# Kernel tuning notes

Measured on AMD Instinct MI355X. Metric: run time of the kernel, lower is better.

The kernel has to match this reference:

```python
import jax, jax.numpy as jnp
import numpy as np

B, S, D = 4, 2048, 2048


def setup_inputs() -> dict:
    key = jax.random.key(0)
    ks = jax.random.split(key, 9)
    scale = 1.0 / np.sqrt(D)
    x = jax.random.normal(ks[0], (B, S, D), dtype=jnp.float32)
    # causal mask, broadcast to [B, S, S]; 0 -> masked
    mask = jnp.broadcast_to(jnp.tril(jnp.ones((S, S), dtype=jnp.int32)), (B, S, S))
    Wq = jax.random.normal(ks[1], (D, D), dtype=jnp.float32) * scale
    Wk = jax.random.normal(ks[2], (D, D), dtype=jnp.float32) * scale
    Wv = jax.random.normal(ks[3], (D, D), dtype=jnp.float32) * scale
    Wp = jax.random.normal(ks[4], (D, D), dtype=jnp.float32) * scale
    bq = jnp.zeros((D,), jnp.float32)
    bk = jnp.zeros((D,), jnp.float32)
    bv = jnp.zeros((D,), jnp.float32)
    bp = jnp.zeros((D,), jnp.float32)
    return {"x": x, "mask": mask, "Wq": Wq, "bq": bq, "Wk": Wk, "bk": bk,
            "Wv": Wv, "bv": bv, "Wp": Wp, "bp": bp}


def reference(x, mask, Wq, bq, Wk, bk, Wv, bv, Wp, bp):
    # single-head scaled dot-product attention (cache=None path, eval mode)
    d_k = x.shape[-1]
    inv_std = 1.0 / jnp.sqrt(jnp.asarray(d_k, x.dtype))
    q = jnp.einsum('bsd,ed->bse', x, Wq) + bq  # nn.Linear: x @ W^T + b
    k = jnp.einsum('bsd,ed->bse', x, Wk) + bk
    v = jnp.einsum('bsd,ed->bse', x, Wv) + bv
    scores = jnp.einsum('bqd,bkd->bqk', q, k) * inv_std  # [B,S,S]
    scores = jnp.where(mask == 0, jnp.asarray(-jnp.inf, scores.dtype), scores)
    attn = jax.nn.softmax(scores, axis=-1)
    ctx = jnp.einsum('bqk,bkd->bqd', attn, v)
    out = jnp.einsum('bsd,ed->bse', ctx, Wp) + bp
    return out
```

## Files before the change

kernel.cpp:

```cpp
#include <hip/hip_runtime.h>
#include <hip/hip_bf16.h>
#include <type_traits>
#include <math.h>


typedef __bf16 bf16x8_t __attribute__((ext_vector_type(8)));
typedef float f32x4_t __attribute__((ext_vector_type(4)));
typedef unsigned short u16x8_t __attribute__((ext_vector_type(8)));

#define BM 128
#define BN 128
#define BK 64

__device__ inline unsigned short f2bf(float f) {
  unsigned int u = __builtin_bit_cast(unsigned int, f);
  unsigned int r = u + 0x7fffu + ((u >> 16) & 1u);
  return (unsigned short)(r >> 16);
}

__device__ inline void gl2lds16(const unsigned short* g, unsigned short* l) {
  __builtin_amdgcn_global_load_lds(
      (const __attribute__((address_space(1))) unsigned int*)g,
      (__attribute__((address_space(3))) unsigned int*)l, 16, 0, 0);
}

__global__ __launch_bounds__(256) void cast_f32_bf16(
    const float* __restrict__ in, unsigned short* __restrict__ out, long n4) {
  long i = blockIdx.x * 256L + threadIdx.x;
  if (i >= n4) return;
  float4 f = ((const float4*)in)[i];
  ushort4 u;
  u.x = f2bf(f.x); u.y = f2bf(f.y); u.z = f2bf(f.z); u.w = f2bf(f.w);
  ((ushort4*)out)[i] = u;
}

__global__ __launch_bounds__(256) void cast_w4(
    const float* __restrict__ w0, const float* __restrict__ w1,
    const float* __restrict__ w2, const float* __restrict__ w3,
    unsigned short* __restrict__ o0, unsigned short* __restrict__ o1,
    unsigned short* __restrict__ o2, unsigned short* __restrict__ o3,
    long n4) {
  long i = blockIdx.x * 256L + threadIdx.x;
  if (i >= n4) return;
  const float* in; unsigned short* out;
  switch (blockIdx.y) {
    case 0: in = w0; out = o0; break;
    case 1: in = w1; out = o1; break;
    case 2: in = w2; out = o2; break;
    default: in = w3; out = o3; break;
  }
  float4 f = ((const float4*)in)[i];
  ushort4 u;
  u.x = f2bf(f.x); u.y = f2bf(f.y); u.z = f2bf(f.z); u.w = f2bf(f.w);
  ((ushort4*)out)[i] = u;
}

#define GEMM_PROLOGUE()                                                        \
  const int tid = threadIdx.x;                                                 \
  const int lane = tid & 63;                                                   \
  const int wave = tid >> 6;                                                   \
  const int wm = (wave >> 1) * 64;                                             \
  const int wn = (wave & 1) * 64;                                              \
  __shared__ unsigned short smem[2 * BM * BK];                      \
  unsigned short* As = smem;                                                   \
  unsigned short* Bs = smem + BM * BK;                                         \
  const int lr = lane >> 3;                                                    \
  const int swcol = ((lane & 7) ^ lr) * 8;                                     \
  const int cbase = wave * 4;                                                  \
  f32x4_t acc[4][4] = {};                                                      \
  const int fr = lane & 15;                                                    \
  const int q4 = lane >> 4;                                                    \
  const int fo0 = ((q4 ^ (fr & 7)) * 8);             \
  const int fo1 = (((q4 + 4) ^ (fr & 7)) * 8);

#define GEMM_KLOOP(Ab, Bb, K, Keff)                                            \
  for (int k0 = 0; k0 < (Keff); k0 += BK) {                                    \
    __syncthreads();                                                           \
    _Pragma("unroll")                                                          \
    for (int i = 0; i < 4; i++) {                                              \
      const int c = cbase + i;                                                 \
      gl2lds16((Ab) + (size_t)(c * 8 + lr) * (K) + k0 + swcol, As + c * 512);  \
      gl2lds16((Bb) + (size_t)(c * 8 + lr) * (K) + k0 + swcol, Bs + c * 512);  \
    }                                                                          \
    __syncthreads();                                                           \
    {                                                                          \
      bf16x8_t af[4], bfv[4];                                                  \
      _Pragma("unroll")                                                        \
      for (int mi = 0; mi < 4; mi++)                                           \
        af[mi] = __builtin_bit_cast(                                           \
            bf16x8_t, *(const u16x8_t*)&As[(wm + mi * 16 + fr) * BK + fo0]);   \
      _Pragma("unroll")                                                        \
      for (int ni = 0; ni < 4; ni++)                                           \
        bfv[ni] = __builtin_bit_cast(                                          \
            bf16x8_t, *(const u16x8_t*)&Bs[(wn + ni * 16 + fr) * BK + fo0]);   \
      _Pragma("unroll")                                                        \
      for (int mi = 0; mi < 4; mi++)                                           \
        _Pragma("unroll")                                                      \
        for (int ni = 0; ni < 4; ni++)                                         \
          acc[mi][ni] = __builtin_amdgcn_mfma_f32_16x16x32_bf16(               \
              af[mi], bfv[ni], acc[mi][ni], 0, 0, 0);                          \
      _Pragma("unroll")                                                        \
      for (int mi = 0; mi < 4; mi++)                                           \
        af[mi] = __builtin_bit_cast(                                           \
            bf16x8_t, *(const u16x8_t*)&As[(wm + mi * 16 + fr) * BK + fo1]);   \
      _Pragma("unroll")                                                        \
      for (int ni = 0; ni < 4; ni++)                                           \
        bfv[ni] = __builtin_bit_cast(                                          \
            bf16x8_t, *(const u16x8_t*)&Bs[(wn + ni * 16 + fr) * BK + fo1]);   \
      _Pragma("unroll")                                                        \
      for (int mi = 0; mi < 4; mi++)                                           \
        _Pragma("unroll")                                                      \
        for (int ni = 0; ni < 4; ni++)                                         \
          acc[mi][ni] = __builtin_amdgcn_mfma_f32_16x16x32_bf16(               \
              af[mi], bfv[ni], acc[mi][ni], 0, 0, 0);                          \
    }                                                                          \
  }

template <int MODE, typename OutT>
__global__ __launch_bounds__(256) void gemm_nt(
    const unsigned short* __restrict__ A, const unsigned short* __restrict__ B,
    OutT* __restrict__ C, const float* __restrict__ bias, float alpha,
    int M, int N, int K, size_t sA, size_t sB, size_t sC) {
  const int bm = blockIdx.y * BM;
  const int bn = blockIdx.x * BN;
  if (MODE == 1 && bn >= bm + BM) return;
  int Keff = K;
  if (MODE == 2) { int kl = bm + BM; Keff = kl < K ? kl : K; }

  A += (size_t)blockIdx.z * sA;
  B += (size_t)blockIdx.z * sB;
  C += (size_t)blockIdx.z * sC;

  GEMM_PROLOGUE();
  const unsigned short* Ab = A + (size_t)bm * K;
  const unsigned short* Bb = B + (size_t)bn * K;
  GEMM_KLOOP(Ab, Bb, K, Keff);

  const int cr = (lane >> 4) * 4;
  const int cc = lane & 15;
#pragma unroll
  for (int ni = 0; ni < 4; ni++) {
    const int col = bn + wn + ni * 16 + cc;
    const float bs = bias ? bias[col] : 0.f;
#pragma unroll
    for (int mi = 0; mi < 4; mi++) {
      const int row = bm + wm + mi * 16 + cr;
#pragma unroll
      for (int r = 0; r < 4; r++) {
        float v = acc[mi][ni][r] * alpha + bs;
        if constexpr (std::is_same_v<OutT, float>)
          C[(size_t)(row + r) * N + col] = v;
        else
          C[(size_t)(row + r) * N + col] = f2bf(v);
      }
    }
  }
}

__global__ __launch_bounds__(256) void gemm_qkv(
    const unsigned short* __restrict__ A, const unsigned short* __restrict__ Bw,
    unsigned short* __restrict__ Q, unsigned short* __restrict__ Kd,
    unsigned short* __restrict__ Vt,
    const float* __restrict__ bq, const float* __restrict__ bk,
    const float* __restrict__ bv, int K, int D, int S) {
  const int bm = blockIdx.y * BM;
  const int bn = blockIdx.x * BN;

  GEMM_PROLOGUE();
  const unsigned short* Ab = A + (size_t)bm * K;
  const unsigned short* Bb = Bw + (size_t)bn * K;
  GEMM_KLOOP(Ab, Bb, K, K);

  const int cr = (lane >> 4) * 4;
  const int cc = lane & 15;
#pragma unroll
  for (int ni = 0; ni < 4; ni++) {
    const int col = bn + wn + ni * 16 + cc;
    const int sel = col >> 11;
    const int idx = col & (D - 1);
    const float bs = (sel == 0 ? bq : sel == 1 ? bk : bv)[idx];
#pragma unroll
    for (int mi = 0; mi < 4; mi++) {
      const int row = bm + wm + mi * 16 + cr;
      if (sel < 2) {
        unsigned short* dst = sel == 0 ? Q : Kd;
#pragma unroll
        for (int r = 0; r < 4; r++)
          dst[(size_t)(row + r) * D + idx] = f2bf(acc[mi][ni][r] + bs);
      } else {
        const int b = row >> 11;
        const int s = row & (S - 1);
        ushort4 pack;
        pack.x = f2bf(acc[mi][ni][0] + bs);
        pack.y = f2bf(acc[mi][ni][1] + bs);
        pack.z = f2bf(acc[mi][ni][2] + bs);
        pack.w = f2bf(acc[mi][ni][3] + bs);
        *(ushort4*)&Vt[(size_t)b * D * S + (size_t)idx * S + s] = pack;
      }
    }
  }
}

__global__ __launch_bounds__(256) void softmax_causal(
    const float* __restrict__ Sc, unsigned short* __restrict__ P, int n) {
  const int row = blockIdx.x;
  const int q = row & (n - 1);
  const float* srow = Sc + (size_t)row * n;
  unsigned short* prow = P + (size_t)row * n;
  const int tid = threadIdx.x, lane = tid & 63, wid = tid >> 6;
  __shared__ float red[4];

  float m = -3.0e38f;
  for (int j = tid; j <= q; j += 256) m = fmaxf(m, srow[j]);
#pragma unroll
  for (int o = 32; o; o >>= 1) m = fmaxf(m, __shfl_down(m, o, 64));
  if (lane == 0) red[wid] = m;
  __syncthreads();
  m = fmaxf(fmaxf(red[0], red[1]), fmaxf(red[2], red[3]));
  __syncthreads();

  float s = 0.f;
  for (int j = tid; j <= q; j += 256) s += __expf(srow[j] - m);
#pragma unroll
  for (int o = 32; o; o >>= 1) s += __shfl_down(s, o, 64);
  if (lane == 0) red[wid] = s;
  __syncthreads();
  s = red[0] + red[1] + red[2] + red[3];
  const float inv = 1.f / s;

  for (int j = tid; j < n; j += 256) {
    float v = (j <= q) ? __expf(srow[j] - m) * inv : 0.f;
    prow[j] = f2bf(v);
  }
}

extern "C" void kernel_launch(void* const* d_in, const int* in_sizes, int n_in,
                              void* d_out, int out_size, void* d_ws, size_t ws_size,
                              hipStream_t stream) {
  const int B = 4, S = 2048, D = 2048;
  const int M = B * S;

  const float* x  = (const float*)d_in[0];
  const float* Wq = (const float*)d_in[2];
  const float* bq = (const float*)d_in[3];
  const float* Wk = (const float*)d_in[4];
  const float* bk = (const float*)d_in[5];
  const float* Wv = (const float*)d_in[6];
  const float* bv = (const float*)d_in[7];
  const float* Wp = (const float*)d_in[8];
  const float* bp = (const float*)d_in[9];
  float* out = (float*)d_out;

  char* ws = (char*)d_ws;
  const size_t MB = 1ull << 20;
  unsigned short* xb   = (unsigned short*)(ws + 0);
  unsigned short* wqkv = (unsigned short*)(ws + 32 * MB);
  unsigned short* wpb  = (unsigned short*)(ws + 56 * MB);
  unsigned short* qb   = (unsigned short*)(ws + 64 * MB);
  unsigned short* kb   = (unsigned short*)(ws + 96 * MB);
  unsigned short* vtb  = (unsigned short*)(ws + 160 * MB);
  float*          sc   = (float*)(ws + 192 * MB);
  unsigned short* pb   = qb;
  unsigned short* cb   = kb;

  const long nx = (long)M * D;
  const long nw = (long)D * D;

  cast_f32_bf16<<<dim3((unsigned)((nx / 4 + 255) / 256)), 256, 0, stream>>>(x, xb, nx / 4);
  cast_w4<<<dim3((unsigned)((nw / 4 + 255) / 256), 4), 256, 0, stream>>>(
      Wq, Wk, Wv, Wp,
      wqkv, wqkv + (size_t)D * D, wqkv + 2 * (size_t)D * D, wpb, nw / 4);

  const dim3 blk(256);

  gemm_qkv<<<dim3(3 * D / BN, M / BM), blk, 0, stream>>>(
      xb, wqkv, qb, kb, vtb, bq, bk, bv, D, D, S);

  const float inv_std = 1.f / sqrtf((float)D);
  gemm_nt<1, float><<<dim3(S / BN, S / BM, B), blk, 0, stream>>>(
      qb, kb, sc, nullptr, inv_std, S, S, D, (size_t)S * D, (size_t)S * D, (size_t)S * S);

  softmax_causal<<<dim3(B * S), blk, 0, stream>>>(sc, pb, S);

  gemm_nt<2, unsigned short><<<dim3(D / BN, S / BM, B), blk, 0, stream>>>(
      pb, vtb, cb, nullptr, 1.f, S, D, S, (size_t)S * S, (size_t)D * S, (size_t)S * D);

  gemm_nt<0, float><<<dim3(D / BN, M / BM), blk, 0, stream>>>(
      cb, wpb, out, bp, 1.f, M, D, D, 0, 0, 0);
}
```

Baseline: 682.9 us.

## Replace 128x128 GEMMs with 256x256 tiles using a double-buffered, interleaved load/MFMA pipeline

Swaps all GEMM kernels for a 256x256 tile, 512-thread version. Each block double-buffers its LDS tiles, interleaving global-to-LDS prefetch of the next K tiles with MFMA compute phases, using explicit waitcnt, sched barriers and setprio. It also remaps workgroup IDs in an XCD-aware way to improve L2 locality. Larger tiles raise data reuse and hide memory latency, at the cost of more registers and 128KB of LDS per block, and of coarser causal skipping in the QK^T and PV GEMMs.

```diff
diff --git a/kernel.cpp b/kernel.cpp
--- a/kernel.cpp
+++ b/kernel.cpp
@@ -8,10 +8,6 @@
 typedef float f32x4_t __attribute__((ext_vector_type(4)));
 typedef unsigned short u16x8_t __attribute__((ext_vector_type(8)));
 
-#define BM 128
-#define BN 128
-#define BK 64
-
 __device__ inline unsigned short f2bf(float f) {
   unsigned int u = __builtin_bit_cast(unsigned int, f);
   unsigned int r = u + 0x7fffu + ((u >> 16) & 1u);
@@ -23,6 +19,19 @@
       (const __attribute__((address_space(1))) unsigned int*)g,
       (__attribute__((address_space(3))) unsigned int*)l, 16, 0, 0);
 }
+
+__device__ __forceinline__ bf16x8_t ldf(const unsigned short* p) {
+  return __builtin_bit_cast(bf16x8_t, *(const u16x8_t*)p);
+}
+
+#define MF(a_, b_, c_) \
+  (c_) = __builtin_amdgcn_mfma_f32_16x16x32_bf16((a_), (b_), (c_), 0, 0, 0)
+#define FENCE() asm volatile("" ::: "memory")
+#define BAR() __builtin_amdgcn_s_barrier()
+#define LGK0() asm volatile("s_waitcnt lgkmcnt(0)" ::: "memory")
+#define VM6() asm volatile("s_waitcnt vmcnt(6)" ::: "memory")
+#define SCHED0() __builtin_amdgcn_sched_barrier(0)
+#define PRIO(x) __builtin_amdgcn_s_setprio(x)
 
 __global__ __launch_bounds__(256) void cast_f32_bf16(
     const float* __restrict__ in, unsigned short* __restrict__ out, long n4) {
@@ -55,99 +64,174 @@
   ((ushort4*)out)[i] = u;
 }
 
-#define GEMM_PROLOGUE()                                                        \
-  const int tid = threadIdx.x;                                                 \
-  const int lane = tid & 63;                                                   \
-  const int wave = tid >> 6;                                                   \
-  const int wm = (wave >> 1) * 64;                                             \
-  const int wn = (wave & 1) * 64;                                              \
-  __shared__ unsigned short smem[2 * BM * BK];                      \
-  unsigned short* As = smem;                                                   \
-  unsigned short* Bs = smem + BM * BK;                                         \
-  const int lr = lane >> 3;                                                    \
-  const int swcol = ((lane & 7) ^ lr) * 8;                                     \
-  const int cbase = wave * 4;                                                  \
-  f32x4_t acc[4][4] = {};                                                      \
-  const int fr = lane & 15;                                                    \
-  const int q4 = lane >> 4;                                                    \
-  const int fo0 = ((q4 ^ (fr & 7)) * 8);             \
-  const int fo1 = (((q4 + 4) ^ (fr & 7)) * 8);
-
-#define GEMM_KLOOP(Ab, Bb, K, Keff)                                            \
-  for (int k0 = 0; k0 < (Keff); k0 += BK) {                                    \
-    __syncthreads();                                                           \
-    _Pragma("unroll")                                                          \
-    for (int i = 0; i < 4; i++) {                                              \
-      const int c = cbase + i;                                                 \
-      gl2lds16((Ab) + (size_t)(c * 8 + lr) * (K) + k0 + swcol, As + c * 512);  \
-      gl2lds16((Bb) + (size_t)(c * 8 + lr) * (K) + k0 + swcol, Bs + c * 512);  \
-    }                                                                          \
-    __syncthreads();                                                           \
-    {                                                                          \
-      bf16x8_t af[4], bfv[4];                                                  \
-      _Pragma("unroll")                                                        \
-      for (int mi = 0; mi < 4; mi++)                                           \
-        af[mi] = __builtin_bit_cast(                                           \
-            bf16x8_t, *(const u16x8_t*)&As[(wm + mi * 16 + fr) * BK + fo0]);   \
-      _Pragma("unroll")                                                        \
-      for (int ni = 0; ni < 4; ni++)                                           \
-        bfv[ni] = __builtin_bit_cast(                                          \
-            bf16x8_t, *(const u16x8_t*)&Bs[(wn + ni * 16 + fr) * BK + fo0]);   \
-      _Pragma("unroll")                                                        \
-      for (int mi = 0; mi < 4; mi++)                                           \
-        _Pragma("unroll")                                                      \
-        for (int ni = 0; ni < 4; ni++)                                         \
-          acc[mi][ni] = __builtin_amdgcn_mfma_f32_16x16x32_bf16(               \
-              af[mi], bfv[ni], acc[mi][ni], 0, 0, 0);                          \
-      _Pragma("unroll")                                                        \
-      for (int mi = 0; mi < 4; mi++)                                           \
-        af[mi] = __builtin_bit_cast(                                           \
-            bf16x8_t, *(const u16x8_t*)&As[(wm + mi * 16 + fr) * BK + fo1]);   \
-      _Pragma("unroll")                                                        \
-      for (int ni = 0; ni < 4; ni++)                                           \
-        bfv[ni] = __builtin_bit_cast(                                          \
-            bf16x8_t, *(const u16x8_t*)&Bs[(wn + ni * 16 + fr) * BK + fo1]);   \
-      _Pragma("unroll")                                                        \
-      for (int mi = 0; mi < 4; mi++)                                           \
-        _Pragma("unroll")                                                      \
-        for (int ni = 0; ni < 4; ni++)                                         \
-          acc[mi][ni] = __builtin_amdgcn_mfma_f32_16x16x32_bf16(               \
-              af[mi], bfv[ni], acc[mi][ni], 0, 0, 0);                          \
-    }                                                                          \
-  }
+__device__ __forceinline__ void g256_kloop(
+    const unsigned short* __restrict__ A, const unsigned short* __restrict__ B,
+    int K, int Keff, unsigned short* smem, f32x4_t (&acc)[8][4]) {
+  const int tid = threadIdx.x;
+  const int lane = tid & 63;
+  const int wave = tid >> 6;
+  const int wr = wave >> 2;
+  const int wc = wave & 3;
+  const int fr = lane & 15;
+  const int q4 = lane >> 4;
+  const int s0 = (q4 ^ (fr & 7)) * 8;
+  const int s1 = ((q4 + 4) ^ (fr & 7)) * 8;
+  const size_t rowK =
+      (size_t)(wave * 8 + (lane >> 3)) * (size_t)K +
+      (size_t)(((lane & 7) ^ ((lane >> 3) & 7)) * 8);
+  const size_t K64 = (size_t)64 * K;
+  const size_t K128 = (size_t)128 * K;
+  const int wofs = wave * 512;
+  const int NT = Keff >> 6;
+
+#define STG(gp_, lh_)                        \
+  do {                                       \
+    const unsigned short* g_ = (gp_) + rowK; \
+    gl2lds16(g_, (lh_) + wofs);              \
+    gl2lds16(g_ + K64, (lh_) + 4096 + wofs); \
+  } while (0)
+
+  STG(A, smem);
+  STG(A + K128, smem + 8192);
+  STG(B, smem + 16384);
+  STG(B + K128, smem + 24576);
+  STG(B + 64, smem + 32768 + 16384);
+  STG(B + K128 + 64, smem + 32768 + 24576);
+  STG(A + 64, smem + 32768);
+  VM6();
+  FENCE();
+  BAR();
+
+  for (int kt = 0; kt < NT; ++kt) {
+    unsigned short* bc = smem + ((kt & 1) << 15);
+    unsigned short* nb = smem + (((kt + 1) & 1) << 15);
+    const unsigned short* Ahc = bc + wr * 8192 + fr * 64;
+    const unsigned short* Bhc =
+        bc + 16384 + (wc >> 1) * 8192 + (wc & 1) * 4096 + fr * 64;
+    int k1 = (kt + 1) << 6; if (k1 >= Keff) k1 -= Keff;
+    int k2 = (kt + 2) << 6; if (k2 >= Keff) k2 -= Keff;
+
+    bf16x8_t bfr[4][2], af01[2][2], af25[4][2], af67[2][2];
+
+#pragma unroll
+    for (int n = 0; n < 4; ++n) {
+      const unsigned short* p = Bhc + n * 1024;
+      bfr[n][0] = ldf(p + s0);
+      bfr[n][1] = ldf(p + s1);
+    }
+#pragma unroll
+    for (int m = 0; m < 2; ++m) {
+      const unsigned short* p = Ahc + m * 1024;
+      af01[m][0] = ldf(p + s0);
+      af01[m][1] = ldf(p + s1);
+    }
+    STG(A + K128 + k1, nb + 8192);
+    FENCE(); BAR(); LGK0(); SCHED0();
+    PRIO(1);
+#pragma unroll
+    for (int m = 0; m < 2; ++m)
+#pragma unroll
+      for (int n = 0; n < 4; ++n) {
+        MF(af01[m][0], bfr[n][0], acc[m][n]);
+        MF(af01[m][1], bfr[n][1], acc[m][n]);
+      }
+    PRIO(0);
+    FENCE(); BAR();
+
+#pragma unroll
+    for (int m = 0; m < 4; ++m) {
+      const unsigned short* p = Ahc + (m + 2) * 1024;
+      af25[m][0] = ldf(p + s0);
+      af25[m][1] = ldf(p + s1);
+    }
+    STG(B + k2, bc + 16384);
+    FENCE(); BAR(); LGK0(); SCHED0();
+    PRIO(1);
+#pragma unroll
+    for (int m = 0; m < 2; ++m)
+#pragma unroll
+      for (int n = 0; n < 4; ++n) {
+        MF(af25[m][0], bfr[n][0], acc[2 + m][n]);
+        MF(af25[m][1], bfr[n][1], acc[2 + m][n]);
+      }
+    PRIO(0);
+    FENCE(); BAR();
+
+#pragma unroll
+    for (int m = 0; m < 2; ++m) {
+      const unsigned short* p = Ahc + (m + 6) * 1024;
+      af67[m][0] = ldf(p + s0);
+      af67[m][1] = ldf(p + s1);
+    }
+    STG(B + K128 + k2, bc + 24576);
+    FENCE(); BAR(); LGK0(); SCHED0();
+    PRIO(1);
+#pragma unroll
+    for (int m = 0; m < 2; ++m)
+#pragma unroll
+      for (int n = 0; n < 4; ++n) {
+        MF(af25[2 + m][0], bfr[n][0], acc[4 + m][n]);
+        MF(af25[2 + m][1], bfr[n][1], acc[4 + m][n]);
+      }
+    PRIO(0);
+    FENCE(); BAR();
+
+    STG(A + k2, bc);
+    FENCE(); BAR(); LGK0(); SCHED0();
+    PRIO(1);
+#pragma unroll
+    for (int m = 0; m < 2; ++m)
+#pragma unroll
+      for (int n = 0; n < 4; ++n) {
+        MF(af67[m][0], bfr[n][0], acc[6 + m][n]);
+        MF(af67[m][1], bfr[n][1], acc[6 + m][n]);
+      }
+    PRIO(0);
+    VM6();
+    FENCE(); BAR();
+  }
+#undef STG
+}
 
 template <int MODE, typename OutT>
-__global__ __launch_bounds__(256) void gemm_nt(
+__global__ __launch_bounds__(512, 2) void gemm256_nt(
     const unsigned short* __restrict__ A, const unsigned short* __restrict__ B,
     OutT* __restrict__ C, const float* __restrict__ bias, float alpha,
-    int M, int N, int K, size_t sA, size_t sB, size_t sC) {
-  const int bm = blockIdx.y * BM;
-  const int bn = blockIdx.x * BN;
-  if (MODE == 1 && bn >= bm + BM) return;
+    int N, int K, size_t sA, size_t sB, size_t sC) {
+  int lin = blockIdx.y * gridDim.x + blockIdx.x;
+  const int nwg = gridDim.x * gridDim.y;
+  lin = (lin & 7) * (nwg >> 3) + (lin >> 3);
+  const int bm = (lin / gridDim.x) * 256;
+  const int bn = (lin % gridDim.x) * 256;
+  if (MODE == 1 && bn >= bm + 256) return;
   int Keff = K;
-  if (MODE == 2) { int kl = bm + BM; Keff = kl < K ? kl : K; }
-
-  A += (size_t)blockIdx.z * sA;
-  B += (size_t)blockIdx.z * sB;
+  if (MODE == 2) { int kl = bm + 256; Keff = kl < K ? kl : K; }
+
+  A += (size_t)blockIdx.z * sA + (size_t)bm * K;
+  B += (size_t)blockIdx.z * sB + (size_t)bn * K;
   C += (size_t)blockIdx.z * sC;
 
-  GEMM_PROLOGUE();
-  const unsigned short* Ab = A + (size_t)bm * K;
-  const unsigned short* Bb = B + (size_t)bn * K;
-  GEMM_KLOOP(Ab, Bb, K, Keff);
-
-  const int cr = (lane >> 4) * 4;
-  const int cc = lane & 15;
-#pragma unroll
-  for (int ni = 0; ni < 4; ni++) {
-    const int col = bn + wn + ni * 16 + cc;
+  __shared__ unsigned short smem[65536];
+  f32x4_t acc[8][4] = {};
+  g256_kloop(A, B, K, Keff, smem, acc);
+
+  const int tid = threadIdx.x;
+  const int lane = tid & 63;
+  const int wave = tid >> 6;
+  const int wr = wave >> 2, wc = wave & 3;
+  const int fr = lane & 15, q4 = lane >> 4;
+  const int r0 = bm + wr * 128 + q4 * 4;
+  const int c0 = bn + wc * 64 + fr;
+#pragma unroll
+  for (int n = 0; n < 4; ++n) {
+    const int col = c0 + n * 16;
     const float bs = bias ? bias[col] : 0.f;
 #pragma unroll
-    for (int mi = 0; mi < 4; mi++) {
-      const int row = bm + wm + mi * 16 + cr;
-#pragma unroll
-      for (int r = 0; r < 4; r++) {
-        float v = acc[mi][ni][r] * alpha + bs;
+    for (int m = 0; m < 8; ++m) {
+      const int row = r0 + m * 16;
+#pragma unroll
+      for (int r = 0; r < 4; ++r) {
+        float v = acc[m][n][r] * alpha + bs;
         if constexpr (std::is_same_v<OutT, float>)
           C[(size_t)(row + r) * N + col] = v;
         else
@@ -157,44 +241,51 @@
   }
 }
 
-__global__ __launch_bounds__(256) void gemm_qkv(
+__global__ __launch_bounds__(512, 2) void gemm256_qkv(
     const unsigned short* __restrict__ A, const unsigned short* __restrict__ Bw,
     unsigned short* __restrict__ Q, unsigned short* __restrict__ Kd,
     unsigned short* __restrict__ Vt,
     const float* __restrict__ bq, const float* __restrict__ bk,
     const float* __restrict__ bv, int K, int D, int S) {
-  const int bm = blockIdx.y * BM;
-  const int bn = blockIdx.x * BN;
-
-  GEMM_PROLOGUE();
-  const unsigned short* Ab = A + (size_t)bm * K;
-  const unsigned short* Bb = Bw + (size_t)bn * K;
-  GEMM_KLOOP(Ab, Bb, K, K);
-
-  const int cr = (lane >> 4) * 4;
-  const int cc = lane & 15;
-#pragma unroll
-  for (int ni = 0; ni < 4; ni++) {
-    const int col = bn + wn + ni * 16 + cc;
+  int lin = blockIdx.y * gridDim.x + blockIdx.x;
+  const int nwg = gridDim.x * gridDim.y;
+  lin = (lin & 7) * (nwg >> 3) + (lin >> 3);
+  const int bm = (lin / gridDim.x) * 256;
+  const int bn = (lin % gridDim.x) * 256;
+
+  __shared__ unsigned short smem[65536];
+  f32x4_t acc[8][4] = {};
+  g256_kloop(A + (size_t)bm * K, Bw + (size_t)bn * K, K, K, smem, acc);
+
+  const int tid = threadIdx.x;
+  const int lane = tid & 63;
+  const int wave = tid >> 6;
+  const int wr = wave >> 2, wc = wave & 3;
+  const int fr = lane & 15, q4 = lane >> 4;
+  const int r0 = bm + wr * 128 + q4 * 4;
+  const int c0 = bn + wc * 64 + fr;
+#pragma unroll
+  for (int n = 0; n < 4; ++n) {
+    const int col = c0 + n * 16;
     const int sel = col >> 11;
     const int idx = col & (D - 1);
     const float bs = (sel == 0 ? bq : sel == 1 ? bk : bv)[idx];
 #pragma unroll
-    for (int mi = 0; mi < 4; mi++) {
-      const int row = bm + wm + mi * 16 + cr;
+    for (int m = 0; m < 8; ++m) {
+      const int row = r0 + m * 16;
       if (sel < 2) {
         unsigned short* dst = sel == 0 ? Q : Kd;
 #pragma unroll
-        for (int r = 0; r < 4; r++)
-          dst[(size_t)(row + r) * D + idx] = f2bf(acc[mi][ni][r] + bs);
+        for (int r = 0; r < 4; ++r)
+          dst[(size_t)(row + r) * D + idx] = f2bf(acc[m][n][r] + bs);
       } else {
         const int b = row >> 11;
         const int s = row & (S - 1);
         ushort4 pack;
-        pack.x = f2bf(acc[mi][ni][0] + bs);
-        pack.y = f2bf(acc[mi][ni][1] + bs);
-        pack.z = f2bf(acc[mi][ni][2] + bs);
-        pack.w = f2bf(acc[mi][ni][3] + bs);
+        pack.x = f2bf(acc[m][n][0] + bs);
+        pack.y = f2bf(acc[m][n][1] + bs);
+        pack.z = f2bf(acc[m][n][2] + bs);
+        pack.w = f2bf(acc[m][n][3] + bs);
         *(ushort4*)&Vt[(size_t)b * D * S + (size_t)idx * S + s] = pack;
       }
     }
@@ -271,20 +362,20 @@
       Wq, Wk, Wv, Wp,
       wqkv, wqkv + (size_t)D * D, wqkv + 2 * (size_t)D * D, wpb, nw / 4);
 
-  const dim3 blk(256);
-
-  gemm_qkv<<<dim3(3 * D / BN, M / BM), blk, 0, stream>>>(
+  const dim3 blk(512);
+
+  gemm256_qkv<<<dim3(3 * D / 256, M / 256), blk, 0, stream>>>(
       xb, wqkv, qb, kb, vtb, bq, bk, bv, D, D, S);
 
   const float inv_std = 1.f / sqrtf((float)D);
-  gemm_nt<1, float><<<dim3(S / BN, S / BM, B), blk, 0, stream>>>(
-      qb, kb, sc, nullptr, inv_std, S, S, D, (size_t)S * D, (size_t)S * D, (size_t)S * S);
-
-  softmax_causal<<<dim3(B * S), blk, 0, stream>>>(sc, pb, S);
-
-  gemm_nt<2, unsigned short><<<dim3(D / BN, S / BM, B), blk, 0, stream>>>(
-      pb, vtb, cb, nullptr, 1.f, S, D, S, (size_t)S * S, (size_t)D * S, (size_t)S * D);
-
-  gemm_nt<0, float><<<dim3(D / BN, M / BM), blk, 0, stream>>>(
-      cb, wpb, out, bp, 1.f, M, D, D, 0, 0, 0);
-}
+  gemm256_nt<1, float><<<dim3(S / 256, S / 256, B), blk, 0, stream>>>(
+      qb, kb, sc, nullptr, inv_std, S, D, (size_t)S * D, (size_t)S * D, (size_t)S * S);
+
+  softmax_causal<<<dim3(B * S), dim3(256), 0, stream>>>(sc, pb, S);
+
+  gemm256_nt<2, unsigned short><<<dim3(D / 256, S / 256, B), blk, 0, stream>>>(
+      pb, vtb, cb, nullptr, 1.f, D, S, (size_t)S * S, (size_t)D * S, (size_t)S * D);
+
+  gemm256_nt<0, float><<<dim3(D / 256, M / 256), blk, 0, stream>>>(
+      cb, wpb, out, bp, 1.f, D, D, 0, 0, 0);
+}
```

Measured after the change: 621.2 us. 9.0% less time.
